# Optimization experiments

Measured on AMD Instinct MI355X. Metric: run time of the kernel, lower is better.

Reference implementation:

```python
import jax, jax.numpy as jnp
import numpy as np

# module constants (from init_kwargs)
R_EQ = 1.0
WELL_DEPTH = 1.0
CUTOFF = 2.5
HEAL = 0.5

N_EDGES = 20_000_000
N_ATOMS = 1_000_000
N_MOL = 1000


def setup_inputs() -> dict:
    key = jax.random.key(0)
    k1, k2 = jax.random.split(key)
    vec_ij = jax.random.normal(k1, (N_EDGES, 3), dtype=jnp.float32)
    positions = jax.random.normal(k2, (N_ATOMS, 3), dtype=jnp.float32)
    idx_i = jax.random.randint(jax.random.fold_in(key, 1), (N_EDGES,), 0, N_ATOMS, dtype=jnp.int32)
    # sorted molecule indices covering [0, N_MOL), last element == N_MOL-1
    idx_m = (jnp.arange(N_ATOMS, dtype=jnp.int32) * N_MOL // N_ATOMS).astype(jnp.int32)
    return {"vec_ij": vec_ij, "positions": positions, "idx_i": idx_i, "idx_m": idx_m}


def reference(vec_ij, positions, idx_i, idx_m):
    # per-edge distance [E,1]
    r = jnp.linalg.norm(vec_ij, axis=1, keepdims=True)
    # CustomCutoff switching function
    t = (r - (CUTOFF - HEAL)) / HEAL
    r_function = 1.0 + t * t * (2.0 * t - 3.0)
    switch = jnp.where(r > CUTOFF - HEAL, r_function, jnp.ones_like(r))
    switch = jnp.where(r > CUTOFF, jnp.zeros_like(r), switch)
    # LJ pair energy
    power_6 = (R_EQ / r) ** 6
    power_12 = power_6 * power_6
    yij = (power_12 - power_6) * switch  # [E,1]
    # scatter-add edges -> atoms
    yi = jax.ops.segment_sum(yij, idx_i, num_segments=positions.shape[0])  # [N,1]
    # index-add atoms -> molecules
    y = jax.ops.segment_sum(yi, idx_m, num_segments=N_MOL)  # [M,1]
    y = jnp.squeeze(y, -1)
    return WELL_DEPTH * 0.5 * y
```

## Files before the change

kernel.cpp:

```cpp
#include <hip/hip_runtime.h>

#define RCUT2  6.25f
#define RIN2   4.0f
#define BT     512

struct __attribute__((aligned(4))) F3 { float x, y, z; };

__global__ __launch_bounds__(256) void init_k(float* __restrict__ out, int n_mol,
                                              int* __restrict__ flag, int flag_init) {
    int i = blockIdx.x * 256 + threadIdx.x;
    if (i < n_mol) out[i] = 0.0f;
    if (i == 0) *flag = flag_init;
}

__global__ __launch_bounds__(256) void build_bounds(
    const int* __restrict__ idx_m, int* __restrict__ start,
    int* __restrict__ flag, int n_atoms, int n_mol) {
    int a = blockIdx.x * 256 + threadIdx.x;
    if (a >= n_atoms) return;
    int m  = idx_m[a];
    int pm = (a == 0) ? -1 : idx_m[a - 1];
    for (int mm = pm + 1; mm <= m; ++mm) start[mm] = a;
    if (a == n_atoms - 1)
        for (int mm = m + 1; mm <= n_mol; ++mm) start[mm] = n_atoms;
    int mf = (int)(((unsigned long long)(unsigned)a * (unsigned)n_mol) / (unsigned)n_atoms);
    if (m != mf) atomicAnd(flag, 0);
}

__global__ __launch_bounds__(BT) void lj_direct(
    const F3*  __restrict__ vec3,
    const int* __restrict__ idx_i,
    const int* __restrict__ bounds_g,
    const int* __restrict__ flag,
    float*     __restrict__ out,
    int n_edges, int n_mol,
    unsigned long long M, int sh)
{
    extern __shared__ float bins[];
    for (int i = threadIdx.x; i < n_mol; i += BT) bins[i] = 0.0f;
    const bool uni = (*flag != 0);
    __syncthreads();

    const int stride = gridDim.x * BT;
    for (int e = blockIdx.x * BT + threadIdx.x; e < n_edges; e += stride) {
        F3  v = vec3[e];
        int a = idx_i[e];

        float r2 = fmaf(v.x, v.x, fmaf(v.y, v.y, v.z * v.z));
        if (r2 > RCUT2) continue;

        float inv2 = __builtin_amdgcn_rcpf(r2);
        float p6   = inv2 * inv2 * inv2;
        float y    = fmaf(p6, p6, -p6);

        float r  = __builtin_amdgcn_sqrtf(r2);
        float t  = fmaf(2.0f, r, -4.0f);
        float sw = fmaf(t * t, fmaf(2.0f, t, -3.0f), 1.0f);
        y *= (r2 > RIN2) ? sw : 1.0f;

        unsigned q = (unsigned)a * (unsigned)n_mol;
        int m = (int)(((unsigned long long)q * M) >> sh);
        if (!uni) {
            if (m > n_mol - 1) m = n_mol - 1;
            if (m < 0) m = 0;
            while (m > 0 && a < bounds_g[m]) --m;
            while (m < n_mol - 1 && a >= bounds_g[m + 1]) ++m;
        }
        atomicAdd(&bins[m], y);
    }

    __syncthreads();
    unsigned off = (blockIdx.x * 131u) % (unsigned)n_mol;
    for (int i = threadIdx.x; i < n_mol; i += BT) {
        int j = i + (int)off; if (j >= n_mol) j -= n_mol;
        float bv = bins[j];
        if (bv != 0.0f) atomicAdd(&out[j], 0.5f * bv);
    }
}

extern "C" void kernel_launch(void* const* d_in, const int* in_sizes, int n_in,
                              void* d_out, int out_size, void* d_ws, size_t ws_size,
                              hipStream_t stream) {
    const float* vec   = (const float*)d_in[0];
    const int*   idx_i = (const int*)d_in[2];
    const int*   idx_m = (const int*)d_in[3];
    float*       out   = (float*)d_out;

    const int n_edges = in_sizes[2];
    const int n_atoms = in_sizes[3];
    const int n_mol   = out_size;

    int* start = (int*)d_ws;
    int* flag  = (int*)d_ws + (n_mol + 2);

    unsigned d = (unsigned)n_atoms;
    unsigned long long M = 1; int sh = 32;
    bool ok = ((unsigned long long)(unsigned)n_mol * d) <= 0x7fffffffull;
    if (ok) {
        bool found = false;
        for (sh = 32; sh <= 62; ++sh) {
            unsigned long long tk = 1ull << sh;
            M = tk / d + 1;
            unsigned long long e = M * d - tk;
            if (e <= (1ull << (sh - 31))) { found = true; break; }
        }
        ok = found;
    }
    if (!ok) { M = 0; sh = 0; }

    init_k<<<(n_mol + 255) / 256, 256, 0, stream>>>(out, n_mol, flag, ok ? 1 : 0);
    build_bounds<<<(n_atoms + 255) / 256, 256, 0, stream>>>(idx_m, start, flag, n_atoms, n_mol);

    const int    nb  = 1024;
    const size_t lds = (size_t)n_mol * sizeof(float);
    lj_direct<<<nb, BT, lds, stream>>>(
        (const F3*)vec, idx_i, start, flag, out, n_edges, n_mol, M, sh);
}
```

Baseline: 400.5 us.

## Vectorize edge loads to float4/int4 and replace global atomics with partial-sum reduction

The edge loop now processes four edges per thread, reading three float4 and one int4 per step instead of unaligned 12-byte structs and scalar indices. When the workspace is large enough, each block writes its per-molecule bins to a partial buffer, and a separate reduction kernel sums them with fewer global atomics. This aims to raise effective load bandwidth and cut contention on the output atomics. It adds an extra kernel launch and about 4 MB of partial traffic, and assumes 16-byte alignment of the inputs.

```diff
diff --git a/kernel.cpp b/kernel.cpp
--- a/kernel.cpp
+++ b/kernel.cpp
@@ -3,8 +3,9 @@
 #define RCUT2  6.25f
 #define RIN2   4.0f
 #define BT     512
-
-struct __attribute__((aligned(4))) F3 { float x, y, z; };
+#define NB     1024
+#define RB     256
+#define RCHUNK 8
 
 __global__ __launch_bounds__(256) void init_k(float* __restrict__ out, int n_mol,
                                               int* __restrict__ flag, int flag_init) {
@@ -27,37 +28,30 @@
     if (m != mf) atomicAnd(flag, 0);
 }
 
-__global__ __launch_bounds__(BT) void lj_direct(
-    const F3*  __restrict__ vec3,
-    const int* __restrict__ idx_i,
-    const int* __restrict__ bounds_g,
-    const int* __restrict__ flag,
-    float*     __restrict__ out,
+__global__ __launch_bounds__(BT) void lj_direct4(
+    const float* __restrict__ vec,
+    const int*   __restrict__ idx_i,
+    const int*   __restrict__ bounds_g,
+    const int*   __restrict__ flag,
+    float*       __restrict__ dest,
     int n_edges, int n_mol,
-    unsigned long long M, int sh)
+    unsigned long long M, int sh, int use_partial)
 {
     extern __shared__ float bins[];
     for (int i = threadIdx.x; i < n_mol; i += BT) bins[i] = 0.0f;
     const bool uni = (*flag != 0);
     __syncthreads();
 
-    const int stride = gridDim.x * BT;
-    for (int e = blockIdx.x * BT + threadIdx.x; e < n_edges; e += stride) {
-        F3  v = vec3[e];
-        int a = idx_i[e];
-
-        float r2 = fmaf(v.x, v.x, fmaf(v.y, v.y, v.z * v.z));
-        if (r2 > RCUT2) continue;
-
+    auto body = [&](float vx, float vy, float vz, int a) {
+        float r2 = fmaf(vx, vx, fmaf(vy, vy, vz * vz));
+        if (r2 > RCUT2) return;
         float inv2 = __builtin_amdgcn_rcpf(r2);
         float p6   = inv2 * inv2 * inv2;
         float y    = fmaf(p6, p6, -p6);
-
         float r  = __builtin_amdgcn_sqrtf(r2);
         float t  = fmaf(2.0f, r, -4.0f);
         float sw = fmaf(t * t, fmaf(2.0f, t, -3.0f), 1.0f);
         y *= (r2 > RIN2) ? sw : 1.0f;
-
         unsigned q = (unsigned)a * (unsigned)n_mol;
         int m = (int)(((unsigned long long)q * M) >> sh);
         if (!uni) {
@@ -67,15 +61,59 @@
             while (m < n_mol - 1 && a >= bounds_g[m + 1]) ++m;
         }
         atomicAdd(&bins[m], y);
+    };
+
+    const float4* __restrict__ vec4 = (const float4*)vec;
+    const int4*   __restrict__ idx4 = (const int4*)idx_i;
+    const int ng     = n_edges >> 2;
+    const int stride = gridDim.x * BT;
+
+    for (int g = blockIdx.x * BT + threadIdx.x; g < ng; g += stride) {
+        float4 va = vec4[3 * g + 0];
+        float4 vb = vec4[3 * g + 1];
+        float4 vc = vec4[3 * g + 2];
+        int4   ia = idx4[g];
+        body(va.x, va.y, va.z, ia.x);
+        body(va.w, vb.x, vb.y, ia.y);
+        body(vb.z, vb.w, vc.x, ia.z);
+        body(vc.y, vc.z, vc.w, ia.w);
+    }
+
+    const int tail = n_edges & 3;
+    if (blockIdx.x == 0 && (int)threadIdx.x < tail) {
+        int e = (ng << 2) + (int)threadIdx.x;
+        body(vec[3 * e + 0], vec[3 * e + 1], vec[3 * e + 2], idx_i[e]);
     }
 
     __syncthreads();
-    unsigned off = (blockIdx.x * 131u) % (unsigned)n_mol;
-    for (int i = threadIdx.x; i < n_mol; i += BT) {
-        int j = i + (int)off; if (j >= n_mol) j -= n_mol;
-        float bv = bins[j];
-        if (bv != 0.0f) atomicAdd(&out[j], 0.5f * bv);
+    if (use_partial) {
+        float* myp = dest + (size_t)blockIdx.x * (size_t)n_mol;
+        for (int i = threadIdx.x; i < n_mol; i += BT) myp[i] = bins[i];
+    } else {
+        unsigned off = (blockIdx.x * 131u) % (unsigned)n_mol;
+        for (int i = threadIdx.x; i < n_mol; i += BT) {
+            int j = i + (int)off; if (j >= n_mol) j -= n_mol;
+            float bv = bins[j];
+            if (bv != 0.0f) atomicAdd(&dest[j], 0.5f * bv);
+        }
     }
+}
+
+__global__ __launch_bounds__(RB) void reduce_k(
+    const float* __restrict__ partial, float* __restrict__ out,
+    int n_mol, int nb)
+{
+    const int colblocks = (n_mol + RB - 1) / RB;
+    const int cb = blockIdx.x % colblocks;
+    const int ch = blockIdx.x / colblocks;
+    const int j  = cb * RB + (int)threadIdx.x;
+    if (j >= n_mol) return;
+    const int rows = nb / RCHUNK;
+    const int b0 = ch * rows, b1 = b0 + rows;
+    float s = 0.0f;
+    #pragma unroll 4
+    for (int b = b0; b < b1; ++b) s += partial[(size_t)b * (size_t)n_mol + j];
+    atomicAdd(&out[j], 0.5f * s);
 }
 
 extern "C" void kernel_launch(void* const* d_in, const int* in_sizes, int n_in,
@@ -90,8 +128,20 @@
     const int n_atoms = in_sizes[3];
     const int n_mol   = out_size;
 
-    int* start = (int*)d_ws;
-    int* flag  = (int*)d_ws + (n_mol + 2);
+    const size_t partial_bytes = (size_t)NB * (size_t)n_mol * sizeof(float);
+    const size_t need = partial_bytes + (size_t)(n_mol + 2) * sizeof(int);
+    const int use_partial = (ws_size >= need) ? 1 : 0;
+
+    float* partial;
+    int*   start;
+    if (use_partial) {
+        partial = (float*)d_ws;
+        start   = (int*)(partial + (size_t)NB * (size_t)n_mol);
+    } else {
+        partial = nullptr;
+        start   = (int*)d_ws;
+    }
+    int* flag = start + (n_mol + 1);
 
     unsigned d = (unsigned)n_atoms;
     unsigned long long M = 1; int sh = 32;
@@ -111,8 +161,14 @@
     init_k<<<(n_mol + 255) / 256, 256, 0, stream>>>(out, n_mol, flag, ok ? 1 : 0);
     build_bounds<<<(n_atoms + 255) / 256, 256, 0, stream>>>(idx_m, start, flag, n_atoms, n_mol);
 
-    const int    nb  = 1024;
     const size_t lds = (size_t)n_mol * sizeof(float);
-    lj_direct<<<nb, BT, lds, stream>>>(
-        (const F3*)vec, idx_i, start, flag, out, n_edges, n_mol, M, sh);
+    lj_direct4<<<NB, BT, lds, stream>>>(
+        vec, idx_i, start, flag,
+        use_partial ? partial : out,
+        n_edges, n_mol, M, sh, use_partial);
+
+    if (use_partial) {
+        const int colblocks = (n_mol + RB - 1) / RB;
+        reduce_k<<<colblocks * RCHUNK, RB, 0, stream>>>(partial, out, n_mol, NB);
+    }
 }
```

Result: slower. 413.3 us (+3.2%).
